# Optimization experiments

Measured on AMD Instinct MI355X. Metric: run time of the kernel, lower is better.

Reference implementation:

```python
import jax, jax.numpy as jnp
import numpy as np

H = 256  # hidden size
I = 2    # input size / output size


def setup_inputs() -> dict:
    key = jax.random.key(0)
    ks = jax.random.split(key, 11)
    s1 = 1.0 / np.sqrt(H)
    u = lambda k, shape: jax.random.uniform(k, shape, jnp.float32, -s1, s1)
    return {
        "inputs": jax.random.normal(ks[0], (512, 256, I), jnp.float32),
        "W_ih1": u(ks[1], (4 * H, I)),
        "W_hh1": u(ks[2], (4 * H, H)),
        "b_ih1": u(ks[3], (4 * H,)),
        "b_hh1": u(ks[4], (4 * H,)),
        "W_ih2": u(ks[5], (4 * H, H)),
        "W_hh2": u(ks[6], (4 * H, H)),
        "b_ih2": u(ks[7], (4 * H,)),
        "b_hh2": u(ks[8], (4 * H,)),
        "W_lin": u(ks[9], (I, H)),
        "b_lin": u(ks[10], (I,)),
    }


def _lstm_cell(x, h, c, W_ih, W_hh, b_ih, b_hh):
    # PyTorch LSTMCell gate order: i, f, g, o
    gates = x @ W_ih.T + b_ih + h @ W_hh.T + b_hh  # (B, 4H)
    i, f, g, o = jnp.split(gates, 4, axis=-1)
    c_new = jax.nn.sigmoid(f) * c + jax.nn.sigmoid(i) * jnp.tanh(g)
    h_new = jax.nn.sigmoid(o) * jnp.tanh(c_new)
    return h_new, c_new


def reference(inputs, W_ih1, W_hh1, b_ih1, b_hh1, W_ih2, W_hh2, b_ih2, b_hh2,
              W_lin, b_lin):
    B = inputs.shape[0]
    xs = jnp.transpose(inputs, (1, 0, 2))  # (T, B, I)
    zeros = jnp.zeros((B, H), inputs.dtype)
    carry0 = (zeros, zeros, zeros, zeros)

    def step(carry, x_t):
        h1, c1, h2, c2 = carry
        # NOTE: the original clones/masks x_t into lstm_input_t but never
        # uses it — the cell consumes raw input_t, so we do the same.
        h1, c1 = _lstm_cell(x_t, h1, c1, W_ih1, W_hh1, b_ih1, b_hh1)
        h2, c2 = _lstm_cell(h1, h2, c2, W_ih2, W_hh2, b_ih2, b_hh2)
        y = h2 @ W_lin.T + b_lin  # (B, I)
        return (h1, c1, h2, c2), y

    _, ys = jax.lax.scan(step, carry0, xs)  # ys: (T, B, I)
    return jnp.transpose(ys, (1, 0, 2))  # (B, T, I)
```

## Files before the change

### kernel.cpp

```cpp
#include <hip/hip_runtime.h>


typedef float vf2 __attribute__((ext_vector_type(2)));
typedef _Float16 vh2 __attribute__((ext_vector_type(2)));
typedef _Float16 vh4 __attribute__((ext_vector_type(4)));
typedef _Float16 vh8 __attribute__((ext_vector_type(8)));

#define NT 512
#define TSTEPS 256
#define NCH 96
#define NSTRM 76
#define NVP 12
#define NLP 8
#define CHB 16384
#define FS 393216

__global__ void prep_kernel(const float* __restrict__ W_ih1,
                            const float* __restrict__ W_hh1,
                            const float* __restrict__ b_ih1,
                            const float* __restrict__ b_hh1,
                            const float* __restrict__ W_ih2,
                            const float* __restrict__ W_hh2,
                            const float* __restrict__ b_ih2,
                            const float* __restrict__ b_hh2,
                            void* __restrict__ ws) {
    const int stride = gridDim.x * blockDim.x;
    const int idx = blockIdx.x * blockDim.x + threadIdx.x;
    _Float16* wh = (_Float16*)ws;
    float* wf = (float*)ws;
    for (int e = idx; e < NCH * 8192; e += stride) {
        int ch = e >> 13, rem = e & 8191;
        int th, r, i;
        if (ch >= NSTRM + NVP) { r = rem >> 12; th = (rem >> 3) & 511; i = rem & 7; }
        else                   { th = rem >> 4; r = (rem >> 3) & 1;    i = rem & 7; }
        int row = th + (r << 9);
        int k = (ch << 3) + i;
        float v;
        if (k < 256)      v = W_hh1[row * 256 + k];
        else if (k < 512) v = W_ih2[row * 256 + (k - 256)];
        else              v = W_hh2[row * 256 + (k - 512)];
        wh[e] = (_Float16)v;
    }
    for (int j = idx; j < 1024; j += stride) {
        wf[FS + j]        = W_ih1[j * 2 + 0];
        wf[FS + 1024 + j] = W_ih1[j * 2 + 1];
        wf[FS + 2048 + j] = b_ih1[j] + b_hh1[j];
        wf[FS + 3072 + j] = b_ih2[j] + b_hh2[j];
    }
}

__device__ __forceinline__ float sig_(float v) {
    return 1.f / (1.f + __expf(-v));
}
__device__ __forceinline__ float tanh_(float v) {
    return 1.f - 2.f / (__expf(2.f * v) + 1.f);
}
__device__ __forceinline__ float fdot2_(vh2 a, vh2 b, float c) {
#if __has_builtin(__builtin_amdgcn_fdot2)
    return __builtin_amdgcn_fdot2(a, b, c, false);
#else
    return c + (float)a.x * (float)b.x + (float)a.y * (float)b.y;
#endif
}

union W8 { vh8 v; vh2 p[4]; };
struct WPair { vh8 r0, r1; };

#define BARRIER() __asm__ volatile("s_waitcnt lgkmcnt(0)\ns_barrier" ::: "memory")

__global__ __launch_bounds__(NT, 2) void lstm_kernel(
    const float* __restrict__ x,
    const void* __restrict__ ws,
    const float* __restrict__ W_lin,
    const float* __restrict__ b_lin,
    float* __restrict__ out)
{
    __shared__ float g1buf[2][1024];
    __shared__ float g2buf[2][1024];
    __shared__ _Float16 h1s[2][256];
    __shared__ _Float16 h2s[2][256];
    __shared__ char lds_park[NLP][CHB];

    const int tid = threadIdx.x;
    const int j = tid;
    const int u = tid & 255, bu = tid >> 8;
    const int b0 = blockIdx.x * 2;
    const char* wstream = (const char*)ws;
    const float* wf = (const float*)ws;

    const float wx0a = wf[FS + j],        wx1a = wf[FS + 1024 + j];
    const float wx0b = wf[FS + 512 + j],  wx1b = wf[FS + 1536 + j];
    const float bj1a = wf[FS + 2048 + j], bj1b = wf[FS + 2560 + j];
    const float bj2a = wf[FS + 3072 + j], bj2b = wf[FS + 3584 + j];

    const int lane = tid & 63, wv = tid >> 6;
    const int ob = (wv >> 1) & 1, oo = wv & 1;
    const float wl0 = W_lin[oo * 256 + 4 * lane + 0];
    const float wl1 = W_lin[oo * 256 + 4 * lane + 1];
    const float wl2 = W_lin[oo * 256 + 4 * lane + 2];
    const float wl3 = W_lin[oo * 256 + 4 * lane + 3];
    const float blin = b_lin[oo];

    ((_Float16*)h1s)[tid] = (_Float16)0.f;
    ((_Float16*)h2s)[tid] = (_Float16)0.f;

    float c1 = 0.f, c2 = 0.f;

    const int t16 = tid * 16, t32 = tid * 32;
    int sp = 0;

    auto loadc = [&](WPair& d) {
        d.r0 = *(const vh8*)(wstream + sp + t32);
        d.r1 = *(const vh8*)(wstream + sp + t32 + 16);
        sp += CHB;
        if (sp == NSTRM * CHB) sp = 0;
    };
    auto usec = [&](const WPair& w, const _Float16 (*hp)[256], int k0,
                    float& A00, float& A01, float& A10, float& A11) {
        W8 u0; u0.v = w.r0;
        W8 u1; u1.v = w.r1;
        W8 ha; ha.v = *(const vh8*)&hp[0][k0];
        W8 hb; hb.v = *(const vh8*)&hp[1][k0];
        A00 = fdot2_(u0.p[0], ha.p[0], A00); A00 = fdot2_(u0.p[1], ha.p[1], A00);
        A00 = fdot2_(u0.p[2], ha.p[2], A00); A00 = fdot2_(u0.p[3], ha.p[3], A00);
        A01 = fdot2_(u0.p[0], hb.p[0], A01); A01 = fdot2_(u0.p[1], hb.p[1], A01);
        A01 = fdot2_(u0.p[2], hb.p[2], A01); A01 = fdot2_(u0.p[3], hb.p[3], A01);
        A10 = fdot2_(u1.p[0], ha.p[0], A10); A10 = fdot2_(u1.p[1], ha.p[1], A10);
        A10 = fdot2_(u1.p[2], ha.p[2], A10); A10 = fdot2_(u1.p[3], ha.p[3], A10);
        A11 = fdot2_(u1.p[0], hb.p[0], A11); A11 = fdot2_(u1.p[1], hb.p[1], A11);
        A11 = fdot2_(u1.p[2], hb.p[2], A11); A11 = fdot2_(u1.p[3], hb.p[3], A11);
    };

    for (int s = 0; s < NLP; ++s) {
        const char* src = wstream + (size_t)(NSTRM + NVP + s) * CHB;
        *(vh8*)&lds_park[s][t16]        = *(const vh8*)(src + t16);
        *(vh8*)&lds_park[s][8192 + t16] = *(const vh8*)(src + 8192 + t16);
    }

    WPair wreg[NVP];
    #pragma unroll
    for (int s = 0; s < NVP; ++s) {
        const char* src = wstream + (size_t)(NSTRM + s) * CHB + t32;
        wreg[s].r0 = *(const vh8*)src;
        wreg[s].r1 = *(const vh8*)(src + 16);
    }

    {
        vf2 x0a = *(const vf2*)(x + (size_t)(b0 + 0) * 512);
        vf2 x0b = *(const vf2*)(x + (size_t)(b0 + 1) * 512);
        g1buf[0][j]       = bj1a + wx0a * x0a.x + wx1a * x0a.y;
        g1buf[1][j]       = bj1a + wx0a * x0b.x + wx1a * x0b.y;
        g1buf[0][512 + j] = bj1b + wx0b * x0a.x + wx1b * x0a.y;
        g1buf[1][512 + j] = bj1b + wx0b * x0b.x + wx1b * x0b.y;
    }
    vf2 xv0 = *(const vf2*)(x + (size_t)(b0 + 0) * 512 + 2);
    vf2 xv1 = *(const vf2*)(x + (size_t)(b0 + 1) * 512 + 2);

    WPair bA, bB, bC, bD;
    loadc(bA); loadc(bB); loadc(bC); loadc(bD);
    __syncthreads();

    auto gemm32 = [&](const _Float16 (*hp)[256],
                      float& A00, float& A01, float& A10, float& A11) {
        #pragma unroll 1
        for (int q = 0; q < 32; q += 4) {
            usec(bA, hp, 8 * q,      A00, A01, A10, A11); loadc(bA);
            usec(bB, hp, 8 * q + 8,  A00, A01, A10, A11); loadc(bB);
            usec(bC, hp, 8 * q + 16, A00, A01, A10, A11); loadc(bC);
            usec(bD, hp, 8 * q + 24, A00, A01, A10, A11); loadc(bD);
        }
    };
    auto gemm12 = [&](const _Float16 (*hp)[256],
                      float& A00, float& A01, float& A10, float& A11) {
        #pragma unroll 1
        for (int q = 0; q < 12; q += 4) {
            usec(bA, hp, 8 * q,      A00, A01, A10, A11); loadc(bA);
            usec(bB, hp, 8 * q + 8,  A00, A01, A10, A11); loadc(bB);
            usec(bC, hp, 8 * q + 16, A00, A01, A10, A11); loadc(bC);
            usec(bD, hp, 8 * q + 24, A00, A01, A10, A11); loadc(bD);
        }
    };

    #pragma unroll 1
    for (int t = 0; t < TSTEPS; ++t) {
        {
            float gi = sig_(g1buf[bu][u]);
            float gf = sig_(g1buf[bu][256 + u]);
            float gg = tanh_(g1buf[bu][512 + u]);
            float go = sig_(g1buf[bu][768 + u]);
            c1 = gf * c1 + gi * gg;
            h1s[bu][u] = (_Float16)(go * tanh_(c1));
        }
        BARRIER();

        if (t > 0 && wv < 4) {
            vh4 hv = *(const vh4*)&h2s[ob][4 * lane];
            float s = (float)hv.x * wl0 + (float)hv.y * wl1
                    + (float)hv.z * wl2 + (float)hv.w * wl3;
            #pragma unroll
            for (int m = 32; m >= 1; m >>= 1) s += __shfl_xor(s, m, 64);
            if (lane == 0)
                out[(size_t)(b0 + ob) * 512 + (t - 1) * 2 + oo] = s + blin;
        }

        float a00 = bj1a + wx0a * xv0.x + wx1a * xv0.y;
        float a01 = bj1a + wx0a * xv1.x + wx1a * xv1.y;
        float a10 = bj1b + wx0b * xv0.x + wx1b * xv0.y;
        float a11 = bj1b + wx0b * xv1.x + wx1b * xv1.y;
        {
            const int tn = (t + 2) & (TSTEPS - 1);
            xv0 = *(const vf2*)(x + (size_t)(b0 + 0) * 512 + tn * 2);
            xv1 = *(const vf2*)(x + (size_t)(b0 + 1) * 512 + tn * 2);
        }
        gemm32(h1s, a00, a01, a10, a11);
        g1buf[0][j] = a00; g1buf[1][j] = a01;
        g1buf[0][512 + j] = a10; g1buf[1][512 + j] = a11;

        a00 = bj2a; a01 = bj2a; a10 = bj2b; a11 = bj2b;
        gemm32(h1s, a00, a01, a10, a11);
        gemm12(h2s, a00, a01, a10, a11);
        #pragma unroll
        for (int s = 0; s < NVP; ++s)
            usec(wreg[s], h2s, 96 + 8 * s, a00, a01, a10, a11);
        #pragma unroll 1
        for (int s = 0; s < NLP; ++s) {
            WPair w;
            w.r0 = *(const vh8*)&lds_park[s][t16];
            w.r1 = *(const vh8*)&lds_park[s][8192 + t16];
            usec(w, h2s, 192 + 8 * s, a00, a01, a10, a11);
        }
        g2buf[0][j] = a00; g2buf[1][j] = a01;
        g2buf[0][512 + j] = a10; g2buf[1][512 + j] = a11;
        BARRIER();

        {
            float gi = sig_(g2buf[bu][u]);
            float gf = sig_(g2buf[bu][256 + u]);
            float gg = tanh_(g2buf[bu][512 + u]);
            float go = sig_(g2buf[bu][768 + u]);
            c2 = gf * c2 + gi * gg;
            h2s[bu][u] = (_Float16)(go * tanh_(c2));
        }
    }

    BARRIER();
    if (wv < 4) {
        vh4 hv = *(const vh4*)&h2s[ob][4 * lane];
        float s = (float)hv.x * wl0 + (float)hv.y * wl1
                + (float)hv.z * wl2 + (float)hv.w * wl3;
        #pragma unroll
        for (int m = 32; m >= 1; m >>= 1) s += __shfl_xor(s, m, 64);
        if (lane == 0)
            out[(size_t)(b0 + ob) * 512 + 255 * 2 + oo] = s + blin;
    }
}

extern "C" void kernel_launch(void* const* d_in, const int* in_sizes, int n_in,
                              void* d_out, int out_size, void* d_ws, size_t ws_size,
                              hipStream_t stream) {
    const float* x     = (const float*)d_in[0];
    const float* W_ih1 = (const float*)d_in[1];
    const float* W_hh1 = (const float*)d_in[2];
    const float* b_ih1 = (const float*)d_in[3];
    const float* b_hh1 = (const float*)d_in[4];
    const float* W_ih2 = (const float*)d_in[5];
    const float* W_hh2 = (const float*)d_in[6];
    const float* b_ih2 = (const float*)d_in[7];
    const float* b_hh2 = (const float*)d_in[8];
    const float* W_lin = (const float*)d_in[9];
    const float* b_lin = (const float*)d_in[10];
    float* out = (float*)d_out;

    prep_kernel<<<256, 256, 0, stream>>>(W_ih1, W_hh1, b_ih1, b_hh1,
                                         W_ih2, W_hh2, b_ih2, b_hh2, d_ws);
    lstm_kernel<<<256, NT, 0, stream>>>(x, d_ws, W_lin, b_lin, out);
}
```

Measured before the change: 3.130 ms.

## Give each thread all four gates of one hidden unit, dropping gate LDS buffers

```diff
diff --git a/kernel.cpp b/kernel.cpp
--- a/kernel.cpp
+++ b/kernel.cpp
@@ -6,12 +6,12 @@
 typedef _Float16 vh4 __attribute__((ext_vector_type(4)));
 typedef _Float16 vh8 __attribute__((ext_vector_type(8)));
 
-#define NT 512
+#define NT 256
 #define TSTEPS 256
 #define NCH 96
-#define NSTRM 76
-#define NVP 12
-#define NLP 8
+#define NSTRM 68
+#define NVP 19
+#define NLP 9
 #define CHB 16384
 #define FS 393216
 
@@ -30,10 +30,8 @@
     float* wf = (float*)ws;
     for (int e = idx; e < NCH * 8192; e += stride) {
         int ch = e >> 13, rem = e & 8191;
-        int th, r, i;
-        if (ch >= NSTRM + NVP) { r = rem >> 12; th = (rem >> 3) & 511; i = rem & 7; }
-        else                   { th = rem >> 4; r = (rem >> 3) & 1;    i = rem & 7; }
-        int row = th + (r << 9);
+        int g = rem >> 11, u = (rem >> 3) & 255, i = rem & 7;
+        int row = (g << 8) + u;
         int k = (ch << 3) + i;
         float v;
         if (k < 256)      v = W_hh1[row * 256 + k];
@@ -64,136 +62,139 @@
 }
 
 union W8 { vh8 v; vh2 p[4]; };
-struct WPair { vh8 r0, r1; };
+struct WQuad { vh8 a, b, c, d; };
 
 #define BARRIER() __asm__ volatile("s_waitcnt lgkmcnt(0)\ns_barrier" ::: "memory")
 
-__global__ __launch_bounds__(NT, 2) void lstm_kernel(
+__global__ __launch_bounds__(NT, 1) void lstm_kernel(
     const float* __restrict__ x,
     const void* __restrict__ ws,
     const float* __restrict__ W_lin,
     const float* __restrict__ b_lin,
     float* __restrict__ out)
 {
-    __shared__ float g1buf[2][1024];
-    __shared__ float g2buf[2][1024];
     __shared__ _Float16 h1s[2][256];
     __shared__ _Float16 h2s[2][256];
     __shared__ char lds_park[NLP][CHB];
 
     const int tid = threadIdx.x;
-    const int j = tid;
-    const int u = tid & 255, bu = tid >> 8;
+    const int u = tid;
     const int b0 = blockIdx.x * 2;
     const char* wstream = (const char*)ws;
-    const float* wf = (const float*)ws;
-
-    const float wx0a = wf[FS + j],        wx1a = wf[FS + 1024 + j];
-    const float wx0b = wf[FS + 512 + j],  wx1b = wf[FS + 1536 + j];
-    const float bj1a = wf[FS + 2048 + j], bj1b = wf[FS + 2560 + j];
-    const float bj2a = wf[FS + 3072 + j], bj2b = wf[FS + 3584 + j];
+    const float* wtab = (const float*)ws;
+
+    const float wxi0 = wtab[FS + u],        wxf0 = wtab[FS + 256 + u];
+    const float wxg0 = wtab[FS + 512 + u],  wxo0 = wtab[FS + 768 + u];
+    const float wxi1 = wtab[FS + 1024 + u], wxf1 = wtab[FS + 1280 + u];
+    const float wxg1 = wtab[FS + 1536 + u], wxo1 = wtab[FS + 1792 + u];
+    const float bi1 = wtab[FS + 2048 + u],  bf1 = wtab[FS + 2304 + u];
+    const float bg1 = wtab[FS + 2560 + u],  bo1 = wtab[FS + 2816 + u];
+    const float bi2 = wtab[FS + 3072 + u],  bf2 = wtab[FS + 3328 + u];
+    const float bg2 = wtab[FS + 3584 + u],  bo2 = wtab[FS + 3840 + u];
 
     const int lane = tid & 63, wv = tid >> 6;
-    const int ob = (wv >> 1) & 1, oo = wv & 1;
+    const int ob = wv >> 1, oo = wv & 1;
     const float wl0 = W_lin[oo * 256 + 4 * lane + 0];
     const float wl1 = W_lin[oo * 256 + 4 * lane + 1];
     const float wl2 = W_lin[oo * 256 + 4 * lane + 2];
     const float wl3 = W_lin[oo * 256 + 4 * lane + 3];
     const float blin = b_lin[oo];
 
-    ((_Float16*)h1s)[tid] = (_Float16)0.f;
-    ((_Float16*)h2s)[tid] = (_Float16)0.f;
-
-    float c1 = 0.f, c2 = 0.f;
-
-    const int t16 = tid * 16, t32 = tid * 32;
+    for (int i = tid; i < 512; i += NT) {
+        ((_Float16*)h1s)[i] = (_Float16)0.f;
+        ((_Float16*)h2s)[i] = (_Float16)0.f;
+    }
+
+    float c1a = 0.f, c1b = 0.f, c2a = 0.f, c2b = 0.f;
+
+    const int t16 = tid * 16;
     int sp = 0;
 
-    auto loadc = [&](WPair& d) {
-        d.r0 = *(const vh8*)(wstream + sp + t32);
-        d.r1 = *(const vh8*)(wstream + sp + t32 + 16);
+    auto loadc = [&](WQuad& d) {
+        const char* p = wstream + sp + t16;
+        d.a = *(const vh8*)p;
+        d.b = *(const vh8*)(p + 4096);
+        d.c = *(const vh8*)(p + 8192);
+        d.d = *(const vh8*)(p + 12288);
         sp += CHB;
         if (sp == NSTRM * CHB) sp = 0;
     };
-    auto usec = [&](const WPair& w, const _Float16 (*hp)[256], int k0,
-                    float& A00, float& A01, float& A10, float& A11) {
-        W8 u0; u0.v = w.r0;
-        W8 u1; u1.v = w.r1;
+    auto usec = [&](const WQuad& w, const _Float16 (*hp)[256], int k0,
+                    float (&A)[8]) {
+        W8 wi; wi.v = w.a;  W8 wff; wff.v = w.b;
+        W8 wg; wg.v = w.c;  W8 wo;  wo.v  = w.d;
         W8 ha; ha.v = *(const vh8*)&hp[0][k0];
         W8 hb; hb.v = *(const vh8*)&hp[1][k0];
-        A00 = fdot2_(u0.p[0], ha.p[0], A00); A00 = fdot2_(u0.p[1], ha.p[1], A00);
-        A00 = fdot2_(u0.p[2], ha.p[2], A00); A00 = fdot2_(u0.p[3], ha.p[3], A00);
-        A01 = fdot2_(u0.p[0], hb.p[0], A01); A01 = fdot2_(u0.p[1], hb.p[1], A01);
-        A01 = fdot2_(u0.p[2], hb.p[2], A01); A01 = fdot2_(u0.p[3], hb.p[3], A01);
-        A10 = fdot2_(u1.p[0], ha.p[0], A10); A10 = fdot2_(u1.p[1], ha.p[1], A10);
-        A10 = fdot2_(u1.p[2], ha.p[2], A10); A10 = fdot2_(u1.p[3], ha.p[3], A10);
-        A11 = fdot2_(u1.p[0], hb.p[0], A11); A11 = fdot2_(u1.p[1], hb.p[1], A11);
-        A11 = fdot2_(u1.p[2], hb.p[2], A11); A11 = fdot2_(u1.p[3], hb.p[3], A11);
+        #pragma unroll
+        for (int m = 0; m < 4; ++m) {
+            A[0] = fdot2_(wi.p[m],  ha.p[m], A[0]);
+            A[1] = fdot2_(wi.p[m],  hb.p[m], A[1]);
+            A[2] = fdot2_(wff.p[m], ha.p[m], A[2]);
+            A[3] = fdot2_(wff.p[m], hb.p[m], A[3]);
+            A[4] = fdot2_(wg.p[m],  ha.p[m], A[4]);
+            A[5] = fdot2_(wg.p[m],  hb.p[m], A[5]);
+            A[6] = fdot2_(wo.p[m],  ha.p[m], A[6]);
+            A[7] = fdot2_(wo.p[m],  hb.p[m], A[7]);
+        }
     };
 
     for (int s = 0; s < NLP; ++s) {
-        const char* src = wstream + (size_t)(NSTRM + NVP + s) * CHB;
-        *(vh8*)&lds_park[s][t16]        = *(const vh8*)(src + t16);
-        *(vh8*)&lds_park[s][8192 + t16] = *(const vh8*)(src + 8192 + t16);
-    }
-
-    WPair wreg[NVP];
+        const char* src = wstream + (size_t)(NSTRM + NVP + s) * CHB + t16;
+        *(vh8*)&lds_park[s][t16]         = *(const vh8*)src;
+        *(vh8*)&lds_park[s][4096 + t16]  = *(const vh8*)(src + 4096);
+        *(vh8*)&lds_park[s][8192 + t16]  = *(const vh8*)(src + 8192);
+        *(vh8*)&lds_park[s][12288 + t16] = *(const vh8*)(src + 12288);
+    }
+
+    WQuad wreg[NVP];
     #pragma unroll
     for (int s = 0; s < NVP; ++s) {
-        const char* src = wstream + (size_t)(NSTRM + s) * CHB + t32;
-        wreg[s].r0 = *(const vh8*)src;
-        wreg[s].r1 = *(const vh8*)(src + 16);
-    }
-
+        const char* src = wstream + (size_t)(NSTRM + s) * CHB + t16;
+        wreg[s].a = *(const vh8*)src;
+        wreg[s].b = *(const vh8*)(src + 4096);
+        wreg[s].c = *(const vh8*)(src + 8192);
+        wreg[s].d = *(const vh8*)(src + 12288);
+    }
+
+    float P[8], Q[8];
     {
         vf2 x0a = *(const vf2*)(x + (size_t)(b0 + 0) * 512);
         vf2 x0b = *(const vf2*)(x + (size_t)(b0 + 1) * 512);
-        g1buf[0][j]       = bj1a + wx0a * x0a.x + wx1a * x0a.y;
-        g1buf[1][j]       = bj1a + wx0a * x0b.x + wx1a * x0b.y;
-        g1buf[0][512 + j] = bj1b + wx0b * x0a.x + wx1b * x0a.y;
-        g1buf[1][512 + j] = bj1b + wx0b * x0b.x + wx1b * x0b.y;
+        P[0] = bi1 + wxi0 * x0a.x + wxi1 * x0a.y;
+        P[1] = bi1 + wxi0 * x0b.x + wxi1 * x0b.y;
+        P[2] = bf1 + wxf0 * x0a.x + wxf1 * x0a.y;
+        P[3] = bf1 + wxf0 * x0b.x + wxf1 * x0b.y;
+        P[4] = bg1 + wxg0 * x0a.x + wxg1 * x0a.y;
+        P[5] = bg1 + wxg0 * x0b.x + wxg1 * x0b.y;
+        P[6] = bo1 + wxo0 * x0a.x + wxo1 * x0a.y;
+        P[7] = bo1 + wxo0 * x0b.x + wxo1 * x0b.y;
     }
     vf2 xv0 = *(const vf2*)(x + (size_t)(b0 + 0) * 512 + 2);
     vf2 xv1 = *(const vf2*)(x + (size_t)(b0 + 1) * 512 + 2);
 
-    WPair bA, bB, bC, bD;
+    WQuad bA, bB, bC, bD;
     loadc(bA); loadc(bB); loadc(bC); loadc(bD);
     __syncthreads();
 
-    auto gemm32 = [&](const _Float16 (*hp)[256],
-                      float& A00, float& A01, float& A10, float& A11) {
+    auto gemm32 = [&](const _Float16 (*hp)[256], float (&A)[8]) {
         #pragma unroll 1
         for (int q = 0; q < 32; q += 4) {
-            usec(bA, hp, 8 * q,      A00, A01, A10, A11); loadc(bA);
-            usec(bB, hp, 8 * q + 8,  A00, A01, A10, A11); loadc(bB);
-            usec(bC, hp, 8 * q + 16, A00, A01, A10, A11); loadc(bC);
-            usec(bD, hp, 8 * q + 24, A00, A01, A10, A11); loadc(bD);
-        }
-    };
-    auto gemm12 = [&](const _Float16 (*hp)[256],
-                      float& A00, float& A01, float& A10, float& A11) {
-        #pragma unroll 1
-        for (int q = 0; q < 12; q += 4) {
-            usec(bA, hp, 8 * q,      A00, A01, A10, A11); loadc(bA);
-            usec(bB, hp, 8 * q + 8,  A00, A01, A10, A11); loadc(bB);
-            usec(bC, hp, 8 * q + 16, A00, A01, A10, A11); loadc(bC);
-            usec(bD, hp, 8 * q + 24, A00, A01, A10, A11); loadc(bD);
+            usec(bA, hp, 8 * q,      A); loadc(bA);
+            usec(bB, hp, 8 * q + 8,  A); loadc(bB);
+            usec(bC, hp, 8 * q + 16, A); loadc(bC);
+            usec(bD, hp, 8 * q + 24, A); loadc(bD);
         }
     };
 
     #pragma unroll 1
     for (int t = 0; t < TSTEPS; ++t) {
-        {
-            float gi = sig_(g1buf[bu][u]);
-            float gf = sig_(g1buf[bu][256 + u]);
-            float gg = tanh_(g1buf[bu][512 + u]);
-            float go = sig_(g1buf[bu][768 + u]);
-            c1 = gf * c1 + gi * gg;
-            h1s[bu][u] = (_Float16)(go * tanh_(c1));
-        }
+        c1a = sig_(P[2]) * c1a + sig_(P[0]) * tanh_(P[4]);
+        c1b = sig_(P[3]) * c1b + sig_(P[1]) * tanh_(P[5]);
+        h1s[0][u] = (_Float16)(sig_(P[6]) * tanh_(c1a));
+        h1s[1][u] = (_Float16)(sig_(P[7]) * tanh_(c1b));
         BARRIER();
 
-        if (t > 0 && wv < 4) {
+        if (t > 0) {
             vh4 hv = *(const vh4*)&h2s[ob][4 * lane];
             float s = (float)hv.x * wl0 + (float)hv.y * wl1
                     + (float)hv.z * wl2 + (float)hv.w * wl3;
@@ -203,48 +204,50 @@
                 out[(size_t)(b0 + ob) * 512 + (t - 1) * 2 + oo] = s + blin;
         }
 
-        float a00 = bj1a + wx0a * xv0.x + wx1a * xv0.y;
-        float a01 = bj1a + wx0a * xv1.x + wx1a * xv1.y;
-        float a10 = bj1b + wx0b * xv0.x + wx1b * xv0.y;
-        float a11 = bj1b + wx0b * xv1.x + wx1b * xv1.y;
+        P[0] = bi1 + wxi0 * xv0.x + wxi1 * xv0.y;
+        P[1] = bi1 + wxi0 * xv1.x + wxi1 * xv1.y;
+        P[2] = bf1 + wxf0 * xv0.x + wxf1 * xv0.y;
+        P[3] = bf1 + wxf0 * xv1.x + wxf1 * xv1.y;
+        P[4] = bg1 + wxg0 * xv0.x + wxg1 * xv0.y;
+        P[5] = bg1 + wxg0 * xv1.x + wxg1 * xv1.y;
+        P[6] = bo1 + wxo0 * xv0.x + wxo1 * xv0.y;
+        P[7] = bo1 + wxo0 * xv1.x + wxo1 * xv1.y;
         {
             const int tn = (t + 2) & (TSTEPS - 1);
             xv0 = *(const vf2*)(x + (size_t)(b0 + 0) * 512 + tn * 2);
             xv1 = *(const vf2*)(x + (size_t)(b0 + 1) * 512 + tn * 2);
         }
-        gemm32(h1s, a00, a01, a10, a11);
-        g1buf[0][j] = a00; g1buf[1][j] = a01;
-        g1buf[0][512 + j] = a10; g1buf[1][512 + j] = a11;
-
-        a00 = bj2a; a01 = bj2a; a10 = bj2b; a11 = bj2b;
-        gemm32(h1s, a00, a01, a10, a11);
-        gemm12(h2s, a00, a01, a10, a11);
+        gemm32(h1s, P);
+
+        Q[0] = bi2; Q[1] = bi2; Q[2] = bf2; Q[3] = bf2;
+        Q[4] = bg2; Q[5] = bg2; Q[6] = bo2; Q[7] = bo2;
+        gemm32(h1s, Q);
+        usec(bA, h2s, 0,  Q); loadc(bA);
+        usec(bB, h2s, 8,  Q); loadc(bB);
+        usec(bC, h2s, 16, Q); loadc(bC);
+        usec(bD, h2s, 24, Q); loadc(bD);
         #pragma unroll
         for (int s = 0; s < NVP; ++s)
-            usec(wreg[s], h2s, 96 + 8 * s, a00, a01, a10, a11);
+            usec(wreg[s], h2s, 32 + 8 * s, Q);
         #pragma unroll 1
         for (int s = 0; s < NLP; ++s) {
-            WPair w;
-            w.r0 = *(const vh8*)&lds_park[s][t16];
-            w.r1 = *(const vh8*)&lds_park[s][8192 + t16];
-            usec(w, h2s, 192 + 8 * s, a00, a01, a10, a11);
-        }
-        g2buf[0][j] = a00; g2buf[1][j] = a01;
-        g2buf[0][512 + j] = a10; g2buf[1][512 + j] = a11;
+            WQuad w;
+            w.a = *(const vh8*)&lds_park[s][t16];
+            w.b = *(const vh8*)&lds_park[s][4096 + t16];
+            w.c = *(const vh8*)&lds_park[s][8192 + t16];
+            w.d = *(const vh8*)&lds_park[s][12288 + t16];
+            usec(w, h2s, 184 + 8 * s, Q);
+        }
         BARRIER();
 
-        {
-            float gi = sig_(g2buf[bu][u]);
-            float gf = sig_(g2buf[bu][256 + u]);
-            float gg = tanh_(g2buf[bu][512 + u]);
-            float go = sig_(g2buf[bu][768 + u]);
-            c2 = gf * c2 + gi * gg;
-            h2s[bu][u] = (_Float16)(go * tanh_(c2));
-        }
+        c2a = sig_(Q[2]) * c2a + sig_(Q[0]) * tanh_(Q[4]);
+        c2b = sig_(Q[3]) * c2b + sig_(Q[1]) * tanh_(Q[5]);
+        h2s[0][u] = (_Float16)(sig_(Q[6]) * tanh_(c2a));
+        h2s[1][u] = (_Float16)(sig_(Q[7]) * tanh_(c2b));
     }
 
     BARRIER();
-    if (wv < 4) {
+    {
         vh4 hv = *(const vh4*)&h2s[ob][4 * lane];
         float s = (float)hv.x * wl0 + (float)hv.y * wl1
                 + (float)hv.z * wl2 + (float)hv.w * wl3;
```

New measurement: 3.313 ms. +5.9%, slower.
